# Optimization experiments

Hardware: AMD Instinct MI355X
Metric: run time of the kernel (lower is better)

The kernel has to match this reference:

```python
import jax, jax.numpy as jnp
import numpy as np

N = 50000
E = 800000
DIM = 256
HEADS = 4
HDIM = DIM // HEADS  # 64
NEG_SLOPE = 0.2
LN_EPS = 1e-5


def _layernorm(x, g, b):
    mu = jnp.mean(x, axis=-1, keepdims=True)
    var = jnp.var(x, axis=-1, keepdims=True)
    return (x - mu) * jax.lax.rsqrt(var + LN_EPS) * g + b


def setup_inputs() -> dict:
    key = jax.random.key(0)
    ks = jax.random.split(key, 10)
    x = jax.random.normal(ks[0], (N, DIM), dtype=jnp.float32)
    edge_index = jax.random.randint(ks[1], (2, E), 0, N, dtype=jnp.int64)
    s = 0.05
    W = jax.random.normal(ks[2], (DIM, DIM), dtype=jnp.float32) * s       # GAT linear (heads*out = dim)
    a_src = jax.random.normal(ks[3], (HEADS, HDIM), dtype=jnp.float32) * s
    a_dst = jax.random.normal(ks[4], (HEADS, HDIM), dtype=jnp.float32) * s
    gat_b = jnp.zeros((DIM,), dtype=jnp.float32)
    ln_g = jnp.ones((DIM,), dtype=jnp.float32)
    ln_b = jnp.zeros((DIM,), dtype=jnp.float32)
    W1 = jax.random.normal(ks[5], (DIM, 4 * DIM), dtype=jnp.float32) * s
    b1 = jnp.zeros((4 * DIM,), dtype=jnp.float32)
    W2 = jax.random.normal(ks[6], (4 * DIM, DIM), dtype=jnp.float32) * s
    b2 = jnp.zeros((DIM,), dtype=jnp.float32)
    return {"x": x, "edge_index": edge_index, "W": W, "a_src": a_src,
            "a_dst": a_dst, "gat_b": gat_b, "ln_g": ln_g, "ln_b": ln_b,
            "W1": W1, "b1": b1, "W2": W2, "b2": b2}


def _gat(x, edge_index, W, a_src, a_dst, gat_b):
    # project and split heads: [N, H, C]
    h = (x @ W).reshape(N, HEADS, HDIM)
    alpha_src = jnp.einsum('nhc,hc->nh', h, a_src)  # [N, H]
    alpha_dst = jnp.einsum('nhc,hc->nh', h, a_dst)  # [N, H]
    src = edge_index[0]
    dst = edge_index[1]
    e = jax.nn.leaky_relu(alpha_src[src] + alpha_dst[dst], NEG_SLOPE)  # [E, H]
    # segment softmax over edges sharing a destination node
    m = jax.ops.segment_max(e, dst, num_segments=N)                   # [N, H]
    ex = jnp.exp(e - m[dst])
    denom = jax.ops.segment_sum(ex, dst, num_segments=N)              # [N, H]
    alpha = ex / (denom[dst] + 1e-16)                                 # [E, H]
    msg = h[src] * alpha[:, :, None]                                  # [E, H, C]
    out = jax.ops.segment_sum(msg.reshape(E, DIM), dst, num_segments=N)
    return out + gat_b


def reference(x, edge_index, W, a_src, a_dst, gat_b, ln_g, ln_b, W1, b1, W2, b2):
    residual = x
    g = _gat(x, edge_index, W, a_src, a_dst, gat_b)
    x = _layernorm(x + g, ln_g, ln_b)
    ffn = jax.nn.gelu(x @ W1 + b1, approximate=False) @ W2 + b2
    x = _layernorm(x + ffn, ln_g, ln_b)  # same norm params reused, as in source
    return x + residual
```

## Files before the change

### kernel.cpp

```cpp
#include <hip/hip_runtime.h>
#include <hip/hip_bf16.h>
#include <math.h>

typedef __bf16 bf16;
typedef bf16 bf16x8 __attribute__((ext_vector_type(8)));
typedef float floatx4 __attribute__((ext_vector_type(4)));

#define NN 50000
#define EE 800000
#define DIMC 256
#define FFC 1024

typedef __attribute__((address_space(3))) unsigned int lds_u32;
typedef __attribute__((address_space(1))) unsigned int gbl_u32;

static __device__ __forceinline__ void glds16(const bf16* g, bf16* l) {
    __builtin_amdgcn_global_load_lds((const gbl_u32*)g, (lds_u32*)l, 16, 0, 0);
}

static __device__ __forceinline__ unsigned short f2b(float f) {
    bf16 b = (bf16)f;
    return __builtin_bit_cast(unsigned short, b);
}
static __device__ __forceinline__ float b2f_lo(unsigned u) { return __uint_as_float(u << 16); }
static __device__ __forceinline__ float b2f_hi(unsigned u) { return __uint_as_float(u & 0xffff0000u); }

static __device__ __forceinline__ float gelu_f(float v) {
    float z = -1.5957691216f * v - 0.0713548163f * v * v * v;
    return v / (1.f + __expf(z));
}

__global__ __launch_bounds__(256)
void k_cast_bf16(const float* __restrict__ in, bf16* __restrict__ out, long n4) {
    long i = (long)blockIdx.x * 256 + threadIdx.x;
    if (i >= n4) return;
    float4 v = ((const float4*)in)[i];
    uint2 p;
    p.x = (unsigned)f2b(v.x) | ((unsigned)f2b(v.y) << 16);
    p.y = (unsigned)f2b(v.z) | ((unsigned)f2b(v.w) << 16);
    ((uint2*)out)[i] = p;
}

__global__ __launch_bounds__(256)
void k_tcast(const float* __restrict__ in, bf16* __restrict__ out, int K, int Nc) {
    __shared__ float t[32][33];
    int n0 = blockIdx.x * 32, k0 = blockIdx.y * 32;
    int tx = threadIdx.x & 31, ty = threadIdx.x >> 5;
#pragma unroll
    for (int i = 0; i < 4; ++i)
        t[ty + i * 8][tx] = in[(long)(k0 + ty + i * 8) * Nc + n0 + tx];
    __syncthreads();
#pragma unroll
    for (int i = 0; i < 4; ++i)
        out[(long)(n0 + ty + i * 8) * K + k0 + tx] = (bf16)t[tx][ty + i * 8];
}

template <int EPI>
__global__ __launch_bounds__(256)
void k_gemmA(const bf16* __restrict__ A, const bf16* __restrict__ BT,
             bf16* __restrict__ C, const float* __restrict__ bias,
             const float* __restrict__ avs, const float* __restrict__ avd,
             float* __restrict__ asrcO, float* __restrict__ adstO,
             int M, int K, int Nc) {
    __shared__ __attribute__((aligned(16))) bf16 smem[17408];
    bf16* As = smem;
    bf16* Bs = smem + 8192;
    const int tid = threadIdx.x;
    const int w = tid >> 6, lane = tid & 63;
    const int gm = blockIdx.x * 128, gn = blockIdx.y * 128;
    const int wm = (w >> 1) * 64, wn = (w & 1) * 64;
    const int lr = lane & 15, lkc = lane >> 4;

    long aoff[4], boff[4];
#pragma unroll
    for (int j = 0; j < 4; ++j) {
        int s = w * 4 + j;
        int r = s * 8 + (lane >> 3);
        int kc = ((lane & 7) ^ (r & 7)) * 8;
        aoff[j] = (long)min(gm + r, M - 1) * K + kc;
        boff[j] = (long)(gn + r) * K + kc;
    }

    floatx4 acc[4][4];
#pragma unroll
    for (int a = 0; a < 4; ++a)
#pragma unroll
        for (int b = 0; b < 4; ++b) acc[a][b] = floatx4{0.f, 0.f, 0.f, 0.f};

    for (int k0 = 0; k0 < K; k0 += 64) {
        if (k0) __syncthreads();
#pragma unroll
        for (int j = 0; j < 4; ++j) {
            int s = w * 4 + j;
            glds16(A + aoff[j] + k0, As + s * 512);
            glds16(BT + boff[j] + k0, Bs + s * 512);
        }
        __syncthreads();
#pragma unroll
        for (int kk = 0; kk < 2; ++kk) {
            bf16x8 af[4], bv[4];
#pragma unroll
            for (int mi = 0; mi < 4; ++mi) {
                int r = wm + mi * 16 + lr;
                int ch = (kk * 4 + lkc) ^ (r & 7);
                af[mi] = *(const bf16x8*)(As + r * 64 + ch * 8);
            }
#pragma unroll
            for (int ni = 0; ni < 4; ++ni) {
                int r = wn + ni * 16 + lr;
                int ch = (kk * 4 + lkc) ^ (r & 7);
                bv[ni] = *(const bf16x8*)(Bs + r * 64 + ch * 8);
            }
#pragma unroll
            for (int mi = 0; mi < 4; ++mi)
#pragma unroll
                for (int ni = 0; ni < 4; ++ni)
                    acc[mi][ni] = __builtin_amdgcn_mfma_f32_16x16x32_bf16(af[mi], bv[ni], acc[mi][ni], 0, 0, 0);
        }
    }

    __syncthreads();
    bf16* cs = smem;
#pragma unroll
    for (int ni = 0; ni < 4; ++ni) {
        const int cl = wn + ni * 16 + lr;
        const float bvs = (EPI == 1) ? bias[gn + cl] : 0.f;
#pragma unroll
        for (int mi = 0; mi < 4; ++mi)
#pragma unroll
            for (int i = 0; i < 4; ++i) {
                int rl = wm + mi * 16 + lkc * 4 + i;
                float v = acc[mi][ni][i] + bvs;
                if (EPI == 1) v = gelu_f(v);
                cs[rl * 136 + cl] = (bf16)v;
            }
    }
    __syncthreads();

    const int c8 = (lane & 15) * 8;
    float as8[8], ad8[8];
    int hd = 0;
    if (EPI == 0) {
        hd = (gn >> 6) + ((lane & 15) >> 3);
        const int cb = hd * 64 + (c8 & 63);
#pragma unroll
        for (int i = 0; i < 8; ++i) { as8[i] = avs[cb + i]; ad8[i] = avd[cb + i]; }
    }

#pragma unroll
    for (int t = 0; t < 8; ++t) {
        int rl = w * 32 + t * 4 + (lane >> 4);
        int grow = gm + rl;
        uint4 val = *(const uint4*)(cs + rl * 136 + c8);
        if (grow < M) *(uint4*)(C + (long)grow * Nc + gn + c8) = val;
        if (EPI == 0) {
            float h0 = b2f_lo(val.x), h1 = b2f_hi(val.x), h2 = b2f_lo(val.y), h3 = b2f_hi(val.y);
            float h4 = b2f_lo(val.z), h5 = b2f_hi(val.z), h6 = b2f_lo(val.w), h7 = b2f_hi(val.w);
            float ds = h0 * as8[0] + h1 * as8[1] + h2 * as8[2] + h3 * as8[3]
                     + h4 * as8[4] + h5 * as8[5] + h6 * as8[6] + h7 * as8[7];
            float dd = h0 * ad8[0] + h1 * ad8[1] + h2 * ad8[2] + h3 * ad8[3]
                     + h4 * ad8[4] + h5 * ad8[5] + h6 * ad8[6] + h7 * ad8[7];
#pragma unroll
            for (int off = 1; off < 8; off <<= 1) { ds += __shfl_xor(ds, off); dd += __shfl_xor(dd, off); }
            if ((lane & 7) == 0 && grow < M) {
                asrcO[grow * 4 + hd] = ds;
                adstO[grow * 4 + hd] = dd;
            }
        }
    }
}

#define STAGE_W(cc, pp) do {                                                    \
    bf16* w1d = smem + (pp) * 8192;                                             \
    bf16* w2d = smem + 16384 + (pp) * 8192;                                     \
    _Pragma("unroll")                                                           \
    for (int j = 0; j < 2; ++j) {                                               \
        int sg = w * 2 + j;                                                     \
        int r = sg * 2 + (lane >> 5);                                           \
        int col = ((lane & 31) ^ (r & 7)) * 8;                                  \
        glds16(W1T + (long)((cc) * 32 + r) * DIMC + col, w1d + sg * 512);       \
    }                                                                           \
    _Pragma("unroll")                                                           \
    for (int j = 0; j < 2; ++j) {                                               \
        int sg = w * 2 + j;                                                     \
        int r = sg * 16 + (lane >> 2);                                          \
        int col = (cc) * 32 + (((lane & 3) ^ ((r >> 1) & 3)) * 8);              \
        glds16(W2T + (long)r * FFC + col, w2d + sg * 512);                      \
    }                                                                           \
} while (0)

__global__ __launch_bounds__(512)
void k_ffn(const bf16* __restrict__ x1b, const bf16* __restrict__ W1T,
           const bf16* __restrict__ W2T, const float* __restrict__ b1,
           const float* __restrict__ b2, const float* __restrict__ x,
           const float* __restrict__ lng, const float* __restrict__ lnb,
           float* __restrict__ out, int M) {
    __shared__ __attribute__((aligned(16))) bf16 smem[38912];
    float* actf = (float*)(smem + 32768);
    float* b1sf = (float*)(smem + 36864);
    const int tid = threadIdx.x;
    const int w = tid >> 6, lane = tid & 63;
    const int lr = lane & 15, lkc = lane >> 4;
    const int mg = w >> 1, nh = w & 1;
    const int gm = blockIdx.x * 64;

    bf16x8 xf[8];
    {
        long rb = (long)min(gm + mg * 16 + lr, M - 1) * DIMC;
#pragma unroll
        for (int kf = 0; kf < 8; ++kf)
            xf[kf] = *(const bf16x8*)(x1b + rb + kf * 32 + lkc * 8);
    }
    if (w < 4) glds16((const bf16*)(b1 + (long)tid * 4), (bf16*)(b1sf + w * 256));
    STAGE_W(0, 0);

    floatx4 accB[8];
#pragma unroll
    for (int i = 0; i < 8; ++i) accB[i] = floatx4{0.f, 0.f, 0.f, 0.f};

    const int rbA = nh * 16 + lr;
    const int rAct = mg * 16 + lr;
    const int kAct = nh * 16 + lr;

#pragma unroll 2
    for (int c = 0; c < 32; ++c) {
        const int p = c & 1;
        const int cn = (c < 31) ? (c + 1) : 31;
        STAGE_W(cn, (c + 1) & 1);
        asm volatile("s_waitcnt vmcnt(4)" ::: "memory");
        __builtin_amdgcn_s_barrier();
        asm volatile("" ::: "memory");

        bf16* w1p = smem + p * 8192;
        bf16* w2p = smem + 16384 + p * 8192;

        floatx4 a0 = floatx4{0.f, 0.f, 0.f, 0.f}, a1 = a0;
#pragma unroll
        for (int kf = 0; kf < 8; kf += 2) {
            int g0 = (kf * 4 + lkc) ^ (rbA & 7);
            int g1 = ((kf + 1) * 4 + lkc) ^ (rbA & 7);
            bf16x8 bva = *(const bf16x8*)(w1p + rbA * 256 + g0 * 8);
            bf16x8 bvb = *(const bf16x8*)(w1p + rbA * 256 + g1 * 8);
            a0 = __builtin_amdgcn_mfma_f32_16x16x32_bf16(xf[kf], bva, a0, 0, 0, 0);
            a1 = __builtin_amdgcn_mfma_f32_16x16x32_bf16(xf[kf + 1], bvb, a1, 0, 0, 0);
        }
        float b1v = b1sf[c * 32 + kAct];
#pragma unroll
        for (int i = 0; i < 4; ++i) {
            int r = mg * 16 + lkc * 4 + i;
            float v = gelu_f(a0[i] + a1[i] + b1v);
            actf[r * 32 + (((kAct >> 2) ^ (r & 7)) << 2) + (kAct & 3)] = v;
        }
        asm volatile("s_waitcnt lgkmcnt(0)" ::: "memory");
        __builtin_amdgcn_s_barrier();
        asm volatile("" ::: "memory");

        {
            int g0 = (lkc * 2) ^ (rAct & 7);
            int g1 = (lkc * 2 + 1) ^ (rAct & 7);
            float4 lo = *(const float4*)(actf + rAct * 32 + g0 * 4);
            float4 hi = *(const float4*)(actf + rAct * 32 + g1 * 4);
            bf16x8 af;
            af[0] = (bf16)lo.x; af[1] = (bf16)lo.y; af[2] = (bf16)lo.z; af[3] = (bf16)lo.w;
            af[4] = (bf16)hi.x; af[5] = (bf16)hi.y; af[6] = (bf16)hi.z; af[7] = (bf16)hi.w;
#pragma unroll
            for (int ni = 0; ni < 8; ++ni) {
                int rb = nh * 128 + ni * 16 + lr;
                int gb = lkc ^ ((rb >> 1) & 3);
                bf16x8 bv = *(const bf16x8*)(w2p + rb * 32 + gb * 8);
                accB[ni] = __builtin_amdgcn_mfma_f32_16x16x32_bf16(af, bv, accB[ni], 0, 0, 0);
            }
        }
        __builtin_amdgcn_s_barrier();
        asm volatile("" ::: "memory");
    }

    __syncthreads();
    bf16* cs = smem;
#pragma unroll
    for (int ni = 0; ni < 8; ++ni) {
        int col = nh * 128 + ni * 16 + lr;
        float b2v = b2[col];
#pragma unroll
        for (int i = 0; i < 4; ++i) {
            int rl = mg * 16 + lkc * 4 + i;
            cs[rl * 264 + col] = (bf16)(accB[ni][i] + b2v);
        }
    }
    __syncthreads();
    float4 g4 = *(const float4*)(lng + lane * 4);
    float4 lb4 = *(const float4*)(lnb + lane * 4);
#pragma unroll 1
    for (int t = 0; t < 8; ++t) {
        int r = w * 8 + t;
        int grow = gm + r;
        long base = (long)min(grow, M - 1) * DIMC + lane * 4;
        uint2 cu = *(const uint2*)(cs + r * 264 + lane * 4);
        uint2 xu = *(const uint2*)(x1b + base);
        float v0 = b2f_lo(cu.x) + b2f_lo(xu.x);
        float v1 = b2f_hi(cu.x) + b2f_hi(xu.x);
        float v2 = b2f_lo(cu.y) + b2f_lo(xu.y);
        float v3 = b2f_hi(cu.y) + b2f_hi(xu.y);
        float s1 = v0 + v1 + v2 + v3;
        float s2 = v0 * v0 + v1 * v1 + v2 * v2 + v3 * v3;
#pragma unroll
        for (int off = 1; off < 64; off <<= 1) { s1 += __shfl_xor(s1, off); s2 += __shfl_xor(s2, off); }
        float mu = s1 * (1.f / DIMC);
        float rs = rsqrtf(s2 * (1.f / DIMC) - mu * mu + 1e-5f);
        float4 xr = *(const float4*)(x + base);
        float4 o;
        o.x = (v0 - mu) * rs * g4.x + lb4.x + xr.x;
        o.y = (v1 - mu) * rs * g4.y + lb4.y + xr.y;
        o.z = (v2 - mu) * rs * g4.z + lb4.z + xr.z;
        o.w = (v3 - mu) * rs * g4.w + lb4.w + xr.w;
        if (grow < M) *(float4*)(out + (long)grow * DIMC + lane * 4) = o;
    }
}

__global__ __launch_bounds__(256)
void k_count(const int* __restrict__ dst, unsigned* __restrict__ deg) {
    int e = blockIdx.x * 256 + threadIdx.x;
    if (e < EE) atomicAdd(&deg[dst[e]], 1u);
}

__global__ __launch_bounds__(1024)
void k_scan(const unsigned* __restrict__ deg, unsigned* __restrict__ rowoff,
            unsigned* __restrict__ cursor) {
    __shared__ unsigned wsum[16], wscan[16];
    __shared__ unsigned carry;
    int tid = threadIdx.x, lane = tid & 63, wid = tid >> 6;
    if (tid == 0) carry = 0;
    __syncthreads();
    for (int base = 0; base < NN; base += 1024) {
        int i = base + tid;
        unsigned v = (i < NN) ? deg[i] : 0u;
        unsigned s = v;
        for (int off = 1; off < 64; off <<= 1) {
            unsigned t = __shfl_up(s, off);
            if (lane >= off) s += t;
        }
        if (lane == 63) wsum[wid] = s;
        __syncthreads();
        if (wid == 0) {
            unsigned t = (lane < 16) ? wsum[lane] : 0u;
            unsigned ts = t;
            for (int off = 1; off < 16; off <<= 1) {
                unsigned u2 = __shfl_up(ts, off);
                if (lane >= off) ts += u2;
            }
            if (lane < 16) wscan[lane] = ts;
        }
        __syncthreads();
        unsigned basew = (wid > 0) ? wscan[wid - 1] : 0u;
        unsigned excl = carry + basew + (s - v);
        if (i < NN) { rowoff[i] = excl; cursor[i] = excl; }
        __syncthreads();
        if (tid == 0) carry += wscan[15];
        __syncthreads();
    }
    if (tid == 0) rowoff[NN] = carry;
}

__global__ __launch_bounds__(256)
void k_fill(const int* __restrict__ src, const int* __restrict__ dst,
            unsigned* __restrict__ cursor, unsigned* __restrict__ elist) {
    int e = blockIdx.x * 256 + threadIdx.x;
    if (e < EE) {
        unsigned p = atomicAdd(&cursor[dst[e]], 1u);
        elist[p] = (unsigned)src[e];
    }
}

__global__ __launch_bounds__(256)
void k_agg_ln1(const unsigned* __restrict__ rowoff, const unsigned* __restrict__ elist,
               const float* __restrict__ asrc, const float* __restrict__ adst,
               const bf16* __restrict__ hb, const float* __restrict__ x,
               const float* __restrict__ gatb, const float* __restrict__ lng,
               const float* __restrict__ lnb, bf16* __restrict__ x1b) {
    int node = (blockIdx.x * 256 + threadIdx.x) >> 6;
    int lane = threadIdx.x & 63;
    if (node >= NN) return;
    int beg = (int)rowoff[node], end = (int)rowoff[node + 1];
    int head = lane >> 4;
    float ad = adst[node * 4 + head];
    const int c = lane * 4;
    const bf16* hc = hb + c;
    const int bl = lane & 48;

    float dsum = 0.f;
    float a0 = 0.f, a1 = 0.f, a2 = 0.f, a3 = 0.f;

    for (int c0 = beg; c0 < end; c0 += 16) {
        int take = end - c0; if (take > 16) take = 16;
        int jj = c0 + (lane & 15);
        float ex = 0.f; int s = 0;
        if (jj < end) {
            s = (int)elist[jj];
            float e = asrc[s * 4 + head] + ad;
            e = (e > 0.f) ? e : 0.2f * e;
            ex = __expf(e);
        }
        dsum += ex;
        if (take == 16) {
#pragma unroll
            for (int j = 0; j < 16; ++j) {
                float al = __shfl(ex, bl + j);
                int sj = __shfl(s, bl + j);
                uint2 u = *(const uint2*)(hc + (long)sj * DIMC);
                a0 += al * b2f_lo(u.x);
                a1 += al * b2f_hi(u.x);
                a2 += al * b2f_lo(u.y);
                a3 += al * b2f_hi(u.y);
            }
        } else {
            for (int j = 0; j < take; ++j) {
                float al = __shfl(ex, bl + j);
                int sj = __shfl(s, bl + j);
                uint2 u = *(const uint2*)(hc + (long)sj * DIMC);
                a0 += al * b2f_lo(u.x);
                a1 += al * b2f_hi(u.x);
                a2 += al * b2f_lo(u.y);
                a3 += al * b2f_hi(u.y);
            }
        }
    }
    dsum += __shfl_xor(dsum, 1);
    dsum += __shfl_xor(dsum, 2);
    dsum += __shfl_xor(dsum, 4);
    dsum += __shfl_xor(dsum, 8);
    float invd = 1.f / (dsum + 1e-16f);
    a0 *= invd; a1 *= invd; a2 *= invd; a3 *= invd;

    long base = (long)node * DIMC + c;
    float4 xr = *(const float4*)(x + base);
    float4 gb = *(const float4*)(gatb + c);
    float v0 = xr.x + a0 + gb.x;
    float v1 = xr.y + a1 + gb.y;
    float v2 = xr.z + a2 + gb.z;
    float v3 = xr.w + a3 + gb.w;
    float s1 = v0 + v1 + v2 + v3;
    float s2 = v0 * v0 + v1 * v1 + v2 * v2 + v3 * v3;
    for (int off = 1; off < 64; off <<= 1) { s1 += __shfl_xor(s1, off); s2 += __shfl_xor(s2, off); }
    float mu = s1 * (1.f / DIMC);
    float rs = rsqrtf(s2 * (1.f / DIMC) - mu * mu + 1e-5f);
    float4 g4 = *(const float4*)(lng + c);
    float4 b4 = *(const float4*)(lnb + c);
    float y0 = (v0 - mu) * rs * g4.x + b4.x;
    float y1 = (v1 - mu) * rs * g4.y + b4.y;
    float y2 = (v2 - mu) * rs * g4.z + b4.z;
    float y3 = (v3 - mu) * rs * g4.w + b4.w;
    uint2 p;
    p.x = (unsigned)f2b(y0) | ((unsigned)f2b(y1) << 16);
    p.y = (unsigned)f2b(y2) | ((unsigned)f2b(y3) << 16);
    *(uint2*)(x1b + base) = p;
}

extern "C" void kernel_launch(void* const* d_in, const int* in_sizes, int n_in,
                              void* d_out, int out_size, void* d_ws, size_t ws_size,
                              hipStream_t stream) {
    const float* x    = (const float*)d_in[0];
    const int*   ei   = (const int*)d_in[1];
    const float* W    = (const float*)d_in[2];
    const float* a_s  = (const float*)d_in[3];
    const float* a_d  = (const float*)d_in[4];
    const float* gatb = (const float*)d_in[5];
    const float* lng  = (const float*)d_in[6];
    const float* lnb  = (const float*)d_in[7];
    const float* W1   = (const float*)d_in[8];
    const float* b1   = (const float*)d_in[9];
    const float* W2   = (const float*)d_in[10];
    const float* b2   = (const float*)d_in[11];
    float* out = (float*)d_out;
    char* ws = (char*)d_ws;

    bf16*     xb     = (bf16*)(ws + 0L);
    bf16*     hb     = (bf16*)(ws + 25600000L);
    bf16*     x1b    = (bf16*)(ws + 51200000L);
    float*    asrc   = (float*)(ws + 179200000L);
    float*    adst   = (float*)(ws + 180000000L);
    unsigned* deg    = (unsigned*)(ws + 180800000L);
    unsigned* cursor = (unsigned*)(ws + 181000192L);
    unsigned* rowoff = (unsigned*)(ws + 181200384L);
    unsigned* elist  = (unsigned*)(ws + 181400832L);
    bf16*     WT     = (bf16*)(ws + 184600832L);
    bf16*     W1T    = (bf16*)(ws + 184731904L);
    bf16*     W2T    = (bf16*)(ws + 185256192L);

    const int* esrc = ei;
    const int* edst = ei + EE;

    hipMemsetAsync(deg, 0, NN * sizeof(unsigned), stream);
    k_cast_bf16<<<12500, 256, 0, stream>>>(x, xb, (long)NN * DIMC / 4);
    {
        dim3 gw(DIMC / 32, DIMC / 32);
        k_tcast<<<gw, 256, 0, stream>>>(W, WT, DIMC, DIMC);
        dim3 gw1(FFC / 32, DIMC / 32);
        k_tcast<<<gw1, 256, 0, stream>>>(W1, W1T, DIMC, FFC);
        dim3 gw2(DIMC / 32, FFC / 32);
        k_tcast<<<gw2, 256, 0, stream>>>(W2, W2T, FFC, DIMC);
    }

    dim3 g1(391, 2);
    k_gemmA<0><<<g1, 256, 0, stream>>>(xb, WT, hb, nullptr, a_s, a_d, asrc, adst, NN, DIMC, DIMC);

    k_count<<<3125, 256, 0, stream>>>(edst, deg);
    k_scan<<<1, 1024, 0, stream>>>(deg, rowoff, cursor);
    k_fill<<<3125, 256, 0, stream>>>(esrc, edst, cursor, elist);

    k_agg_ln1<<<12500, 256, 0, stream>>>(rowoff, elist, asrc, adst, hb, x, gatb, lng, lnb, x1b);

    k_ffn<<<782, 512, 0, stream>>>(x1b, W1T, W2T, b1, b2, x, lng, lnb, out, NN);
}
```

Baseline: 530.3 us.

## Load FFN weights directly from global memory instead of LDS double-buffering

The FFN kernel no longer stages W1/W2 chunks and b1 into LDS through a double-buffered global_load_lds pipeline. Each wave now reads its MFMA B operands straight from global memory (relying on L2/cache reuse across blocks), and LDS shrinks to the activation and output tile. Launch bounds request 4 waves per SIMD for higher occupancy. The trade-off is losing the explicit prefetch overlap and LDS reuse across waves, in exchange for fewer barriers and less LDS pressure.

```diff
diff --git a/kernel.cpp b/kernel.cpp
--- a/kernel.cpp
+++ b/kernel.cpp
@@ -170,34 +170,14 @@
     }
 }
 
-#define STAGE_W(cc, pp) do {                                                    \
-    bf16* w1d = smem + (pp) * 8192;                                             \
-    bf16* w2d = smem + 16384 + (pp) * 8192;                                     \
-    _Pragma("unroll")                                                           \
-    for (int j = 0; j < 2; ++j) {                                               \
-        int sg = w * 2 + j;                                                     \
-        int r = sg * 2 + (lane >> 5);                                           \
-        int col = ((lane & 31) ^ (r & 7)) * 8;                                  \
-        glds16(W1T + (long)((cc) * 32 + r) * DIMC + col, w1d + sg * 512);       \
-    }                                                                           \
-    _Pragma("unroll")                                                           \
-    for (int j = 0; j < 2; ++j) {                                               \
-        int sg = w * 2 + j;                                                     \
-        int r = sg * 16 + (lane >> 2);                                          \
-        int col = (cc) * 32 + (((lane & 3) ^ ((r >> 1) & 3)) * 8);              \
-        glds16(W2T + (long)r * FFC + col, w2d + sg * 512);                      \
-    }                                                                           \
-} while (0)
-
-__global__ __launch_bounds__(512)
+__global__ __launch_bounds__(512, 4)
 void k_ffn(const bf16* __restrict__ x1b, const bf16* __restrict__ W1T,
            const bf16* __restrict__ W2T, const float* __restrict__ b1,
            const float* __restrict__ b2, const float* __restrict__ x,
            const float* __restrict__ lng, const float* __restrict__ lnb,
            float* __restrict__ out, int M) {
-    __shared__ __attribute__((aligned(16))) bf16 smem[38912];
-    float* actf = (float*)(smem + 32768);
-    float* b1sf = (float*)(smem + 36864);
+    __shared__ __attribute__((aligned(16))) bf16 smem[16896];
+    float* actf = (float*)smem;
     const int tid = threadIdx.x;
     const int w = tid >> 6, lane = tid & 63;
     const int lr = lane & 15, lkc = lane >> 4;
@@ -211,8 +191,6 @@
         for (int kf = 0; kf < 8; ++kf)
             xf[kf] = *(const bf16x8*)(x1b + rb + kf * 32 + lkc * 8);
     }
-    if (w < 4) glds16((const bf16*)(b1 + (long)tid * 4), (bf16*)(b1sf + w * 256));
-    STAGE_W(0, 0);
 
     floatx4 accB[8];
 #pragma unroll
@@ -221,39 +199,27 @@
     const int rbA = nh * 16 + lr;
     const int rAct = mg * 16 + lr;
     const int kAct = nh * 16 + lr;
-
-#pragma unroll 2
+    const bf16* w1p = W1T + (long)rbA * DIMC + lkc * 8;
+    const bf16* w2p = W2T + (long)(nh * 128 + lr) * FFC + lkc * 8;
+
     for (int c = 0; c < 32; ++c) {
-        const int p = c & 1;
-        const int cn = (c < 31) ? (c + 1) : 31;
-        STAGE_W(cn, (c + 1) & 1);
-        asm volatile("s_waitcnt vmcnt(4)" ::: "memory");
-        __builtin_amdgcn_s_barrier();
-        asm volatile("" ::: "memory");
-
-        bf16* w1p = smem + p * 8192;
-        bf16* w2p = smem + 16384 + p * 8192;
-
+        const bf16* w1c = w1p + (long)c * 32 * DIMC;
         floatx4 a0 = floatx4{0.f, 0.f, 0.f, 0.f}, a1 = a0;
 #pragma unroll
         for (int kf = 0; kf < 8; kf += 2) {
-            int g0 = (kf * 4 + lkc) ^ (rbA & 7);
-            int g1 = ((kf + 1) * 4 + lkc) ^ (rbA & 7);
-            bf16x8 bva = *(const bf16x8*)(w1p + rbA * 256 + g0 * 8);
-            bf16x8 bvb = *(const bf16x8*)(w1p + rbA * 256 + g1 * 8);
+            bf16x8 bva = *(const bf16x8*)(w1c + kf * 32);
+            bf16x8 bvb = *(const bf16x8*)(w1c + (kf + 1) * 32);
             a0 = __builtin_amdgcn_mfma_f32_16x16x32_bf16(xf[kf], bva, a0, 0, 0, 0);
             a1 = __builtin_amdgcn_mfma_f32_16x16x32_bf16(xf[kf + 1], bvb, a1, 0, 0, 0);
         }
-        float b1v = b1sf[c * 32 + kAct];
+        float b1v = b1[c * 32 + kAct];
 #pragma unroll
         for (int i = 0; i < 4; ++i) {
             int r = mg * 16 + lkc * 4 + i;
             float v = gelu_f(a0[i] + a1[i] + b1v);
             actf[r * 32 + (((kAct >> 2) ^ (r & 7)) << 2) + (kAct & 3)] = v;
         }
-        asm volatile("s_waitcnt lgkmcnt(0)" ::: "memory");
-        __builtin_amdgcn_s_barrier();
-        asm volatile("" ::: "memory");
+        __syncthreads();
 
         {
             int g0 = (lkc * 2) ^ (rAct & 7);
@@ -263,19 +229,16 @@
             bf16x8 af;
             af[0] = (bf16)lo.x; af[1] = (bf16)lo.y; af[2] = (bf16)lo.z; af[3] = (bf16)lo.w;
             af[4] = (bf16)hi.x; af[5] = (bf16)hi.y; af[6] = (bf16)hi.z; af[7] = (bf16)hi.w;
+            const bf16* w2c = w2p + c * 32;
 #pragma unroll
             for (int ni = 0; ni < 8; ++ni) {
-                int rb = nh * 128 + ni * 16 + lr;
-                int gb = lkc ^ ((rb >> 1) & 3);
-                bf16x8 bv = *(const bf16x8*)(w2p + rb * 32 + gb * 8);
+                bf16x8 bv = *(const bf16x8*)(w2c + (long)ni * 16 * FFC);
                 accB[ni] = __builtin_amdgcn_mfma_f32_16x16x32_bf16(af, bv, accB[ni], 0, 0, 0);
             }
         }
-        __builtin_amdgcn_s_barrier();
-        asm volatile("" ::: "memory");
-    }
-
-    __syncthreads();
+        __syncthreads();
+    }
+
     bf16* cs = smem;
 #pragma unroll
     for (int ni = 0; ni < 8; ++ni) {
```

Result: slower. 818.1 us (+54.3%).
